# Kernel optimization log

Measured on AMD Instinct MI355X. Metric: run time of the kernel, lower is better.

## Reference

```python
import jax, jax.numpy as jnp
import numpy as np

B, L, NV = 16, 512, 64
D = 512
PATCH_LEN, STRIDE, PADDING = 16, 8, 8
N_PATCH = (L - PATCH_LEN) // STRIDE + 2  # 64
PRED = 192
MEM = 8192
TOPK = 8
NHEAD = 4
NORM_CONST = 0.4
HEAD_NF = D * N_PATCH


def _pos_emb(n, d):
    pos = np.arange(n)[:, None].astype(np.float32)
    div = np.exp(np.arange(0, d, 2).astype(np.float32) * (-np.log(10000.0) / d))
    pe = np.zeros((n, d), np.float32)
    pe[:, 0::2] = np.sin(pos * div)
    pe[:, 1::2] = np.cos(pos * div)
    return jnp.asarray(pe)

POS = _pos_emb(N_PATCH, D)


def gelu(x):
    return jax.nn.gelu(x, approximate=False)  # torch nn.GELU default = exact erf


def setup_inputs() -> dict:
    key = jax.random.key(0)
    ks = jax.random.split(key, 16)
    s = lambda i, shape, scale=0.02: jax.random.normal(ks[i], shape, jnp.float32) * scale
    return dict(
        x_enc=jax.random.normal(ks[0], (B, L, NV), jnp.float32),
        W_val=s(1, (PATCH_LEN, D), 0.05),
        mem_bank=s(2, (MEM, D), 1.0),
        W_m1=s(3, (D, 2 * D)), b_m1=jnp.zeros((2 * D,), jnp.float32),
        W_m2=s(4, (2 * D, D)), b_m2=jnp.zeros((D,), jnp.float32),
        W_q=s(5, (D, D)), b_q=jnp.zeros((D,), jnp.float32),
        W_k=s(6, (D, D)), b_k=jnp.zeros((D,), jnp.float32),
        W_v=s(7, (D, D)), b_v=jnp.zeros((D,), jnp.float32),
        W_o=s(8, (D, D)), b_o=jnp.zeros((D,), jnp.float32),
        W_g1=s(9, (2 * D, D)), b_g1=jnp.zeros((D,), jnp.float32),
        W_g2=s(10, (D, 2)), b_g2=jnp.zeros((2,), jnp.float32),
        W_h=s(11, (HEAD_NF, PRED)), b_h=jnp.zeros((PRED,), jnp.float32),
        W_f1=s(12, (PRED, 2 * PRED)), b_f1=jnp.zeros((2 * PRED,), jnp.float32),
        W_f2=s(13, (2 * PRED, PRED)), b_f2=jnp.zeros((PRED,), jnp.float32),
    )


def reference(x_enc, W_val, mem_bank, W_m1, b_m1, W_m2, b_m2,
              W_q, b_q, W_k, b_k, W_v, b_v, W_o, b_o,
              W_g1, b_g1, W_g2, b_g2, W_h, b_h, W_f1, b_f1, W_f2, b_f2):
    # instance normalization over the time axis (means detached in torch)
    means = jax.lax.stop_gradient(jnp.mean(x_enc, axis=1, keepdims=True))
    xc = x_enc - means
    stdev = jnp.sqrt(jnp.var(xc, axis=1, keepdims=True) + 1e-5) / NORM_CONST
    x = xc / stdev                                              # [B, L, NV]

    # patch embedding: replication pad at end, unfold, linear + sinusoidal pos
    xt = jnp.transpose(x, (0, 2, 1))                            # [B, NV, L]
    xt = jnp.concatenate([xt, jnp.repeat(xt[..., -1:], PADDING, axis=-1)], axis=-1)
    win = (jnp.arange(N_PATCH) * STRIDE)[:, None] + jnp.arange(PATCH_LEN)  # [N, P]
    patches = xt[..., win].reshape(B * NV, N_PATCH, PATCH_LEN)  # [BN, N, P]
    emb = patches @ W_val + POS                                 # [BN, N, D]

    # local memory: mean-pooled query -> matmul similarity -> top-k gather -> MLP
    qflat = jnp.mean(emb, axis=1)                               # [BN, D]
    sim = qflat @ mem_bank.T                                    # [BN, MEM]
    _, idx = jax.lax.top_k(sim, TOPK)                           # [BN, K]
    retr = mem_bank[idx]                                        # [BN, K, D]
    h = gelu(retr @ W_m1 + b_m1) @ W_m2 + b_m2
    local = jnp.mean(h, axis=1, keepdims=True) + emb            # [BN, N, D]

    # global memory: multihead self-attention (4 heads, batch_first)
    dh = D // NHEAD
    heads = lambda t: t.reshape(B * NV, N_PATCH, NHEAD, dh).transpose(0, 2, 1, 3)
    q = heads(emb @ W_q + b_q)
    k = heads(emb @ W_k + b_k)
    v = heads(emb @ W_v + b_v)
    att = jax.nn.softmax(jnp.einsum('bhqd,bhkd->bhqk', q, k) / jnp.sqrt(jnp.float32(dh)), axis=-1)
    glob = jnp.einsum('bhqk,bhkd->bhqd', att, v).transpose(0, 2, 1, 3).reshape(B * NV, N_PATCH, D)
    glob = glob @ W_o + b_o                                     # [BN, N, D]

    # gated fusion of local/global memory
    comb = jnp.concatenate([local, glob], axis=-1)              # [BN, N, 2D]
    gate = jax.nn.softmax(gelu(comb @ W_g1 + b_g1) @ W_g2 + b_g2, axis=-1)
    mem = gate[..., 0:1] * local + gate[..., 1:2] * glob        # [BN, N, D]

    # flatten -> memory head -> fusion layer with residual
    flat = mem.reshape(B * NV, HEAD_NF)
    mh = (flat @ W_h + b_h).reshape(B, NV, PRED)
    pred = gelu(gelu(mh @ W_f1 + b_f1) @ W_f2 + b_f2) + mh
    pred = jnp.transpose(pred, (0, 2, 1))                       # [B, PRED, NV]

    # denormalize
    return pred * stdev + means
```

## Files before the change

### kernel.cpp

```cpp
#include <hip/hip_runtime.h>
#include <stdint.h>

#define DEV __device__ __forceinline__

typedef uint16_t u16;
typedef __bf16 bf16x8 __attribute__((ext_vector_type(8)));
typedef float f32x4 __attribute__((ext_vector_type(4)));
typedef u16 u16x8 __attribute__((ext_vector_type(8)));
typedef u16 u16x4 __attribute__((ext_vector_type(4)));

DEV float bf2f(u16 v) { return __uint_as_float(((uint32_t)v) << 16); }
DEV u16 f2bf(float f) {
  uint32_t u = __float_as_uint(f);
  u += 0x7fffu + ((u >> 16) & 1u);
  return (u16)(u >> 16);
}
DEV float gelu_f(float x) { return 0.5f * x * (1.0f + erff(x * 0.7071067811865475f)); }

DEV void gload_lds16(const u16* g, u16* l) {
  __builtin_amdgcn_global_load_lds(
      (const __attribute__((address_space(1))) void*)g,
      (__attribute__((address_space(3))) void*)l, 16, 0, 0);
}

struct __align__(16) Scratch {
  float POSb[64 * 512];
  float meanv[1024];
  float stdv[1024];
  float mh[1024 * 192];
  int idxB[8192];
  float qflat[1024 * 512];
  float gatel[65536 * 2];
  u16 hmeanB[1024 * 512];
  u16 gmeanB[1024 * 1024];
  u16 WqT[512 * 512];
  u16 WkT[512 * 512];
  u16 WvT[512 * 512];
  u16 WoT[512 * 512];
  u16 Wm1T[1024 * 512];
  u16 Wm2T[512 * 1024];
  u16 Wg1T[512 * 1024];
  u16 WhT[256 * 32768];
  u16 memdupB[8192 * 1536];
  u16 embh[65536 * 512];
  u16 qb[65536 * 512];
  u16 kb[65536 * 512];
  u16 vb[65536 * 512];
};
__device__ Scratch g_s;

__global__ __launch_bounds__(256) void zerof_kernel(float* __restrict__ p, int n) {
  int t = blockIdx.x * 256 + threadIdx.x;
  if (t < n) p[t] = 0.f;
}
__global__ __launch_bounds__(256) void zerou_kernel(u16* __restrict__ p, int n) {
  int t = blockIdx.x * 256 + threadIdx.x;
  if (t < n) p[t] = 0;
}

__global__ __launch_bounds__(256) void pos_kernel(float* __restrict__ POS) {
  int n = blockIdx.x;
  int i = threadIdx.x;
  float div = expf((float)(2 * i) * (-9.210340371976184f / 512.0f));
  float arg = (float)n * div;
  POS[n * 512 + 2 * i] = sinf(arg);
  POS[n * 512 + 2 * i + 1] = cosf(arg);
}

__global__ __launch_bounds__(256) void stats_kernel(const float* __restrict__ x_enc,
                                                    float* __restrict__ meanv,
                                                    float* __restrict__ stdv) {
  int b = blockIdx.x;
  int v = threadIdx.x & 63;
  int g = threadIdx.x >> 6;
  float s = 0.f, s2 = 0.f;
  for (int l = g; l < 512; l += 4) {
    float x = x_enc[((long)b * 512 + l) * 64 + v];
    s += x; s2 += x * x;
  }
  __shared__ float sh[2][4][64];
  sh[0][g][v] = s; sh[1][g][v] = s2;
  __syncthreads();
  if (g == 0) {
    s = sh[0][0][v] + sh[0][1][v] + sh[0][2][v] + sh[0][3][v];
    s2 = sh[1][0][v] + sh[1][1][v] + sh[1][2][v] + sh[1][3][v];
    float mu = s * (1.f / 512.f);
    float var = s2 * (1.f / 512.f) - mu * mu;
    meanv[b * 64 + v] = mu;
    stdv[b * 64 + v] = sqrtf(var + 1e-5f) * 2.5f;
  }
}

__global__ __launch_bounds__(256) void transpose_kernel(const float* __restrict__ in,
                                                        u16* __restrict__ out, int R, int C) {
  __shared__ u16 t[32][33];
  int bx = blockIdx.x * 32;
  int by = blockIdx.y * 32;
  int tx = threadIdx.x & 31, ty = threadIdx.x >> 5;
  for (int i = ty; i < 32; i += 8) t[i][tx] = f2bf(in[(long)(by + i) * C + bx + tx]);
  __syncthreads();
  for (int i = ty; i < 32; i += 8) out[(long)(bx + i) * R + by + tx] = t[tx][i];
}

__global__ __launch_bounds__(256) void emb_kernel(const float* __restrict__ x_enc,
                                                  const float* __restrict__ W_val,
                                                  const float* __restrict__ POS,
                                                  const float* __restrict__ meanv,
                                                  const float* __restrict__ stdv,
                                                  u16* __restrict__ embh,
                                                  float* __restrict__ qflat) {
  int bn = blockIdx.x;
  int b = bn >> 6, v = bn & 63;
  int tid = threadIdx.x;
  __shared__ __align__(16) float wv[16 * 512];
  __shared__ __align__(16) float pt[64 * 16];
  for (int i = tid; i < 8192; i += 256) wv[i] = W_val[i];
  float mu = meanv[bn];
  float inv = 1.f / stdv[bn];
  for (int i = tid; i < 1024; i += 256) {
    int n = i >> 4, p = i & 15;
    int l = n * 8 + p; if (l > 511) l = 511;
    pt[i] = (x_enc[((long)b * 512 + l) * 64 + v] - mu) * inv;
  }
  __syncthreads();
  float qs0 = 0.f, qs1 = 0.f;
  int d0 = tid, d1 = tid + 256;
  for (int n = 0; n < 64; ++n) {
    float a0 = POS[n * 512 + d0], a1 = POS[n * 512 + d1];
#pragma unroll
    for (int p = 0; p < 16; ++p) {
      float pv = pt[n * 16 + p];
      a0 += pv * wv[p * 512 + d0];
      a1 += pv * wv[p * 512 + d1];
    }
    long base = ((long)bn * 64 + n) * 512;
    embh[base + d0] = f2bf(a0);
    embh[base + d1] = f2bf(a1);
    qs0 += a0; qs1 += a1;
  }
  qflat[(long)bn * 512 + d0] = qs0 * (1.f / 64.f);
  qflat[(long)bn * 512 + d1] = qs1 * (1.f / 64.f);
}

__global__ __launch_bounds__(256) void qsplit_kernel(const float* __restrict__ qflat,
                                                     u16* __restrict__ qsC) {
  int t = blockIdx.x * 256 + threadIdx.x;
  int bn = t >> 9, d = t & 511;
  float q = qflat[t];
  u16 hi = f2bf(q);
  u16 lo = f2bf(q - bf2f(hi));
  long base = (long)bn * 1536;
  qsC[base + d] = hi;
  qsC[base + 512 + d] = lo;
  qsC[base + 1024 + d] = hi;
}

__global__ __launch_bounds__(256) void memdup_kernel(const float* __restrict__ mb,
                                                     u16* __restrict__ md) {
  int t = blockIdx.x * 256 + threadIdx.x;
  int n = t >> 9, k = t & 511;
  float m = mb[t];
  u16 hi = f2bf(m);
  u16 lo = f2bf(m - bf2f(hi));
  long base = (long)n * 1536;
  md[base + k] = hi;
  md[base + 512 + k] = hi;
  md[base + 1024 + k] = lo;
}

template <int EPI>
__global__ __launch_bounds__(256) void gemm_nt(const u16* __restrict__ Ag,
                                               const u16* __restrict__ Bt,
                                               const float* __restrict__ bias,
                                               void* __restrict__ C,
                                               int lda, int ldb, int K, int Nreal, int ldc) {
  __shared__ __align__(16) u16 As[128 * 64];
  __shared__ __align__(16) u16 Bs[128 * 64];
  const int tid = threadIdx.x;
  const long bm = (long)blockIdx.x * 128;
  const long bnn = (long)blockIdx.y * 128;
  const long koff = (long)blockIdx.z * K;
  const int lane = tid & 63;
  const int w = tid >> 6;
  const int wm = (w & 1) * 64;
  const int wn = (w >> 1) * 64;
  const int r16 = lane & 15;
  const int q4 = lane >> 4;

  f32x4 acc[4][4] = {};

  const u16* ap[4];
  const u16* bp[4];
  u16* al[4];
  u16* bl[4];
#pragma unroll
  for (int j = 0; j < 4; ++j) {
    int cid = (j * 4 + w) * 64 + lane;
    int r = cid >> 3;
    int g = (cid & 7) ^ (r & 7);
    ap[j] = Ag + (bm + r) * lda + koff + g * 8;
    bp[j] = Bt + (bnn + r) * ldb + koff + g * 8;
    al[j] = As + cid * 8;
    bl[j] = Bs + cid * 8;
  }

  for (int k0 = 0; k0 < K; k0 += 64) {
#pragma unroll
    for (int j = 0; j < 4; ++j) gload_lds16(ap[j] + k0, al[j]);
#pragma unroll
    for (int j = 0; j < 4; ++j) gload_lds16(bp[j] + k0, bl[j]);
    __syncthreads();
#pragma unroll
    for (int sub = 0; sub < 2; ++sub) {
      const int gg = q4 + sub * 4;
      bf16x8 av[4], bv[4];
#pragma unroll
      for (int i = 0; i < 4; ++i) {
        int r = wm + i * 16 + r16;
        av[i] = *reinterpret_cast<const bf16x8*>(As + (r * 8 + (gg ^ (r & 7))) * 8);
      }
#pragma unroll
      for (int j2 = 0; j2 < 4; ++j2) {
        int r = wn + j2 * 16 + r16;
        bv[j2] = *reinterpret_cast<const bf16x8*>(Bs + (r * 8 + (gg ^ (r & 7))) * 8);
      }
#pragma unroll
      for (int i = 0; i < 4; ++i)
#pragma unroll
        for (int j2 = 0; j2 < 4; ++j2)
          acc[i][j2] = __builtin_amdgcn_mfma_f32_16x16x32_bf16(av[i], bv[j2], acc[i][j2], 0, 0, 0);
    }
    __syncthreads();
  }

#pragma unroll
  for (int i = 0; i < 4; ++i)
#pragma unroll
    for (int j = 0; j < 4; ++j)
#pragma unroll
      for (int r = 0; r < 4; ++r) {
        long grow = bm + wm + i * 16 + q4 * 4 + r;
        int gcol = (int)bnn + wn + j * 16 + r16;
        float v = acc[i][j][r];
        if (gcol < Nreal) {
          if (EPI == 0 || EPI == 1) {
            v += bias[gcol];
            if (EPI == 1) v = gelu_f(v);
            ((u16*)C)[grow * ldc + gcol] = f2bf(v);
          } else if (EPI == 2) {
            atomicAdd((float*)C + grow * ldc + gcol, v);
          } else {
            ((float*)C)[grow * ldc + gcol] = v;
          }
        }
      }
}

DEV bool better(float v1, int i1, float v2, int i2) {
  return v1 > v2 || (v1 == v2 && i1 < i2);
}
__global__ __launch_bounds__(256) void topk_kernel(const float* __restrict__ sim,
                                                   int* __restrict__ idxout) {
  const int bn = blockIdx.x;
  const int tid = threadIdx.x;
  const float* row = sim + (long)bn * 8192;
  float bv[8]; int bi[8];
#pragma unroll
  for (int r = 0; r < 8; ++r) { bv[r] = -3.0e38f; bi[r] = 0x7fffffff; }
  for (int n = tid; n < 8192; n += 256) {
    float v = row[n];
    if (better(v, n, bv[7], bi[7])) {
      bv[7] = v; bi[7] = n;
      for (int r = 7; r > 0; --r) {
        if (!better(bv[r], bi[r], bv[r - 1], bi[r - 1])) break;
        float tv = bv[r]; bv[r] = bv[r - 1]; bv[r - 1] = tv;
        int ti = bi[r]; bi[r] = bi[r - 1]; bi[r - 1] = ti;
      }
    }
  }
  __shared__ float lv[256 * 8];
  __shared__ int li[256 * 8];
#pragma unroll
  for (int r = 0; r < 8; ++r) { lv[tid * 8 + r] = bv[r]; li[tid * 8 + r] = bi[r]; }
  __syncthreads();
  for (int step = 128; step >= 1; step >>= 1) {
    if (tid < step) {
      float av[8], xv[8]; int ai[8], xi[8];
#pragma unroll
      for (int r = 0; r < 8; ++r) {
        av[r] = lv[tid * 8 + r]; ai[r] = li[tid * 8 + r];
        xv[r] = lv[(tid + step) * 8 + r]; xi[r] = li[(tid + step) * 8 + r];
      }
      int ia = 0, ib = 0;
      float mv[8]; int mi[8];
#pragma unroll
      for (int r = 0; r < 8; ++r) {
        if (better(av[ia], ai[ia], xv[ib], xi[ib])) { mv[r] = av[ia]; mi[r] = ai[ia]; ++ia; }
        else { mv[r] = xv[ib]; mi[r] = xi[ib]; ++ib; }
      }
#pragma unroll
      for (int r = 0; r < 8; ++r) { lv[tid * 8 + r] = mv[r]; li[tid * 8 + r] = mi[r]; }
    }
    __syncthreads();
  }
  if (tid < 8) idxout[bn * 8 + tid] = li[tid];
}

__global__ __launch_bounds__(256) void gather_kernel(const float* __restrict__ mb,
                                                     const int* __restrict__ idx,
                                                     u16* __restrict__ retrB) {
  int t = blockIdx.x * 256 + threadIdx.x;
  int m = t >> 6;
  int c8 = (t & 63) * 8;
  long r = idx[m];
  if (r < 0) r = 0;
  if (r > 8191) r = 8191;
  const float* src = mb + r * 512 + c8;
  u16* dst = retrB + (long)m * 512 + c8;
#pragma unroll
  for (int z = 0; z < 8; ++z) dst[z] = f2bf(src[z]);
}

__global__ __launch_bounds__(256) void gmean_kernel(const u16* __restrict__ hid,
                                                    u16* __restrict__ gmeanB) {
  int t = blockIdx.x * 256 + threadIdx.x;
  int bn = t >> 10, j = t & 1023;
  float s = 0.f;
#pragma unroll
  for (int k = 0; k < 8; ++k) s += bf2f(hid[(long)(bn * 8 + k) * 1024 + j]);
  gmeanB[t] = f2bf(s * 0.125f);
}

__global__ __launch_bounds__(256) void attn_kernel(u16* __restrict__ qb,
                                                   const u16* __restrict__ kb,
                                                   const u16* __restrict__ vb) {
  __shared__ __align__(16) u16 smem[26752];
  u16* Qs = smem;
  u16* Ks = smem + 8704;
  float* ss = (float*)(smem + 8704);
  u16* ps = smem;
  u16* Vb = smem + 17408;
  float* red = (float*)(smem + 25728);
  const int bn = blockIdx.x, h = blockIdx.y;
  const int tid = threadIdx.x;
  const int lane = tid & 63, w = tid >> 6;
  const int r16 = lane & 15, q4 = lane >> 4;
  const long base = (long)bn * 64 * 512 + h * 128;

  for (int c = tid; c < 1024; c += 256) {
    int r = c >> 4, c8 = (c & 15) * 8;
    u16x8 vq = *(const u16x8*)(qb + base + (long)r * 512 + c8);
    u16x8 vk = *(const u16x8*)(kb + base + (long)r * 512 + c8);
    u16x8 vv = *(const u16x8*)(vb + base + (long)r * 512 + c8);
    *(u16x8*)(Qs + r * 136 + c8) = vq;
    *(u16x8*)(Ks + r * 136 + c8) = vk;
    int kt = r >> 5, q4t = (r >> 3) & 3, e = r & 7;
    int nt = c8 >> 4, rb = c8 & 15;
    int vbase = (nt * 2 + kt) * 520 + (q4t * 16 + rb) * 8 + e;
#pragma unroll
    for (int z = 0; z < 8; ++z) Vb[vbase + z * 8] = vv[z];
  }
  __syncthreads();

  const int m0 = w * 16;
  f32x4 accS[4] = {};
#pragma unroll
  for (int k0 = 0; k0 < 128; k0 += 32) {
    bf16x8 av = *(const bf16x8*)(Qs + (m0 + r16) * 136 + k0 + q4 * 8);
#pragma unroll
    for (int j = 0; j < 4; ++j) {
      bf16x8 bvf = *(const bf16x8*)(Ks + (j * 16 + r16) * 136 + k0 + q4 * 8);
      accS[j] = __builtin_amdgcn_mfma_f32_16x16x32_bf16(av, bvf, accS[j], 0, 0, 0);
    }
  }
  __syncthreads();
  const float scale = 0.08838834764831845f;
#pragma unroll
  for (int j = 0; j < 4; ++j)
#pragma unroll
    for (int r = 0; r < 4; ++r)
      ss[(m0 + q4 * 4 + r) * 66 + j * 16 + r16] = accS[j][r] * scale;
  __syncthreads();

  {
    int r = tid >> 2, p = tid & 3;
    float* row = ss + r * 66 + p * 16;
    float mx = -3.0e38f;
#pragma unroll
    for (int c2 = 0; c2 < 16; ++c2) mx = fmaxf(mx, row[c2]);
    red[r * 4 + p] = mx;
    __syncthreads();
    float m4 = fmaxf(fmaxf(red[r * 4], red[r * 4 + 1]),
                     fmaxf(red[r * 4 + 2], red[r * 4 + 3]));
    float s = 0.f;
#pragma unroll
    for (int c2 = 0; c2 < 16; ++c2) {
      float e = expf(row[c2] - m4);
      row[c2] = e;
      s += e;
    }
    red[256 + r * 4 + p] = s;
    __syncthreads();
    float inv = 1.f / (red[256 + r * 4] + red[256 + r * 4 + 1] +
                       red[256 + r * 4 + 2] + red[256 + r * 4 + 3]);
    u16x8 o0, o1;
#pragma unroll
    for (int z = 0; z < 8; ++z) {
      o0[z] = f2bf(row[z] * inv);
      o1[z] = f2bf(row[8 + z] * inv);
    }
    *(u16x8*)(ps + r * 72 + p * 16) = o0;
    *(u16x8*)(ps + r * 72 + p * 16 + 8) = o1;
  }
  __syncthreads();

  bf16x8 av0 = *(const bf16x8*)(ps + (m0 + r16) * 72 + q4 * 8);
  bf16x8 av1 = *(const bf16x8*)(ps + (m0 + r16) * 72 + 32 + q4 * 8);
#pragma unroll
  for (int nt = 0; nt < 8; ++nt) {
    f32x4 accO = {};
    bf16x8 bv0 = *(const bf16x8*)(Vb + (nt * 2 + 0) * 520 + lane * 8);
    bf16x8 bv1 = *(const bf16x8*)(Vb + (nt * 2 + 1) * 520 + lane * 8);
    accO = __builtin_amdgcn_mfma_f32_16x16x32_bf16(av0, bv0, accO, 0, 0, 0);
    accO = __builtin_amdgcn_mfma_f32_16x16x32_bf16(av1, bv1, accO, 0, 0, 0);
    int d = nt * 16 + r16;
#pragma unroll
    for (int r = 0; r < 4; ++r) {
      int i = m0 + q4 * 4 + r;
      qb[base + (long)i * 512 + d] = f2bf(accO[r]);
    }
  }
}

__global__ __launch_bounds__(256) void local_kernel(u16* __restrict__ embh,
                                                    const u16* __restrict__ hmeanB) {
  long t = (long)blockIdx.x * 256 + threadIdx.x;
  long m = t >> 9;
  int d = (int)(t & 511);
  int bn = (int)(m >> 6);
  embh[t] = f2bf(bf2f(hmeanB[(long)bn * 512 + d]) + bf2f(embh[t]));
}

__global__ __launch_bounds__(256) void gemm_cat(const u16* __restrict__ A1,
                                                const u16* __restrict__ A2,
                                                const u16* __restrict__ Bt,
                                                const float* __restrict__ bias,
                                                u16* __restrict__ C) {
  __shared__ __align__(16) u16 As[128 * 64];
  __shared__ __align__(16) u16 Bs[128 * 64];
  const int tid = threadIdx.x;
  const long bm = (long)blockIdx.x * 128;
  const long bnn = (long)blockIdx.y * 128;
  const int lane = tid & 63;
  const int w = tid >> 6;
  const int wm = (w & 1) * 64;
  const int wn = (w >> 1) * 64;
  const int r16 = lane & 15;
  const int q4 = lane >> 4;

  f32x4 acc[4][4] = {};

  const u16* ap1[4];
  const u16* ap2[4];
  const u16* bp[4];
  u16* al[4];
  u16* bl[4];
#pragma unroll
  for (int j = 0; j < 4; ++j) {
    int cid = (j * 4 + w) * 64 + lane;
    int r = cid >> 3;
    int g = (cid & 7) ^ (r & 7);
    ap1[j] = A1 + (bm + r) * 512 + g * 8;
    ap2[j] = A2 + (bm + r) * 512 + g * 8;
    bp[j] = Bt + (bnn + r) * 1024 + g * 8;
    al[j] = As + cid * 8;
    bl[j] = Bs + cid * 8;
  }

  for (int k0 = 0; k0 < 1024; k0 += 64) {
    if (k0 < 512) {
#pragma unroll
      for (int j = 0; j < 4; ++j) gload_lds16(ap1[j] + k0, al[j]);
    } else {
#pragma unroll
      for (int j = 0; j < 4; ++j) gload_lds16(ap2[j] + (k0 - 512), al[j]);
    }
#pragma unroll
    for (int j = 0; j < 4; ++j) gload_lds16(bp[j] + k0, bl[j]);
    __syncthreads();
#pragma unroll
    for (int sub = 0; sub < 2; ++sub) {
      const int gg = q4 + sub * 4;
      bf16x8 av[4], bv[4];
#pragma unroll
      for (int i = 0; i < 4; ++i) {
        int r = wm + i * 16 + r16;
        av[i] = *reinterpret_cast<const bf16x8*>(As + (r * 8 + (gg ^ (r & 7))) * 8);
      }
#pragma unroll
      for (int j2 = 0; j2 < 4; ++j2) {
        int r = wn + j2 * 16 + r16;
        bv[j2] = *reinterpret_cast<const bf16x8*>(Bs + (r * 8 + (gg ^ (r & 7))) * 8);
      }
#pragma unroll
      for (int i = 0; i < 4; ++i)
#pragma unroll
        for (int j2 = 0; j2 < 4; ++j2)
          acc[i][j2] = __builtin_amdgcn_mfma_f32_16x16x32_bf16(av[i], bv[j2], acc[i][j2], 0, 0, 0);
    }
    __syncthreads();
  }

#pragma unroll
  for (int i = 0; i < 4; ++i)
#pragma unroll
    for (int j = 0; j < 4; ++j)
#pragma unroll
      for (int r = 0; r < 4; ++r) {
        long grow = bm + wm + i * 16 + q4 * 4 + r;
        int gcol = (int)bnn + wn + j * 16 + r16;
        float v = acc[i][j][r] + bias[gcol];
        C[grow * 512 + gcol] = f2bf(gelu_f(v));
      }
}

__global__ __launch_bounds__(256) void g2_kernel(const u16* __restrict__ h1b,
                                                 const float* __restrict__ W_g2,
                                                 const float* __restrict__ b_g2,
                                                 float* __restrict__ gatel) {
  int m = blockIdx.x * 4 + (threadIdx.x >> 6);
  int lane = threadIdx.x & 63;
  const u16* row = h1b + (long)m * 512;
  float a0 = 0.f, a1 = 0.f;
  for (int i = lane; i < 512; i += 64) {
    float h = bf2f(row[i]);
    a0 += h * W_g2[i * 2];
    a1 += h * W_g2[i * 2 + 1];
  }
  for (int off = 32; off; off >>= 1) {
    a0 += __shfl_down(a0, off);
    a1 += __shfl_down(a1, off);
  }
  if (lane == 0) {
    a0 += b_g2[0];
    a1 += b_g2[1];
    float mx = fmaxf(a0, a1);
    float e0 = expf(a0 - mx), e1 = expf(a1 - mx);
    float inv = 1.f / (e0 + e1);
    gatel[(long)m * 2] = e0 * inv;
    gatel[(long)m * 2 + 1] = e1 * inv;
  }
}

__global__ __launch_bounds__(256) void memc_kernel(const u16* __restrict__ localB,
                                                   const u16* __restrict__ globB,
                                                   const float* __restrict__ gatel,
                                                   u16* __restrict__ memB) {
  long t = (long)blockIdx.x * 256 + threadIdx.x;
  long m = t >> 9;
  float loc = bf2f(localB[t]);
  float gl = bf2f(globB[t]);
  float g0 = gatel[m * 2], g1 = gatel[m * 2 + 1];
  memB[t] = f2bf(g0 * loc + g1 * gl);
}

__global__ __launch_bounds__(256) void fusion_kernel(const float* __restrict__ mh,
                                                     const float* __restrict__ b_h,
                                                     const float* __restrict__ W_f1,
                                                     const float* __restrict__ b_f1,
                                                     const float* __restrict__ W_f2,
                                                     const float* __restrict__ b_f2,
                                                     const float* __restrict__ meanv,
                                                     const float* __restrict__ stdv,
                                                     float* __restrict__ out) {
  int bn = blockIdx.x;
  int tid = threadIdx.x;
  __shared__ float mrow[192];
  __shared__ float h1[384];
  if (tid < 192) mrow[tid] = mh[(long)bn * 192 + tid] + b_h[tid];
  __syncthreads();
  for (int j = tid; j < 384; j += 256) {
    float a = b_f1[j];
    for (int i = 0; i < 192; ++i) a += mrow[i] * W_f1[i * 384 + j];
    h1[j] = gelu_f(a);
  }
  __syncthreads();
  if (tid < 192) {
    float a = b_f2[tid];
    for (int j = 0; j < 384; ++j) a += h1[j] * W_f2[j * 192 + tid];
    float o = gelu_f(a) + mrow[tid];
    int b = bn >> 6, v = bn & 63;
    out[((long)b * 192 + tid) * 64 + v] = o * stdv[bn] + meanv[bn];
  }
}

extern "C" void kernel_launch(void* const* d_in, const int* in_sizes, int n_in,
                              void* d_out, int out_size, void* d_ws, size_t ws_size,
                              hipStream_t stream) {
  (void)in_sizes; (void)n_in; (void)out_size; (void)d_ws; (void)ws_size;
  const float* x_enc = (const float*)d_in[0];
  const float* W_val = (const float*)d_in[1];
  const float* mem_bank = (const float*)d_in[2];
  const float* W_m1 = (const float*)d_in[3];
  const float* b_m1 = (const float*)d_in[4];
  const float* W_m2 = (const float*)d_in[5];
  const float* b_m2 = (const float*)d_in[6];
  const float* W_q = (const float*)d_in[7];
  const float* b_q = (const float*)d_in[8];
  const float* W_k = (const float*)d_in[9];
  const float* b_k = (const float*)d_in[10];
  const float* W_v = (const float*)d_in[11];
  const float* b_v = (const float*)d_in[12];
  const float* W_o = (const float*)d_in[13];
  const float* b_o = (const float*)d_in[14];
  const float* W_g1 = (const float*)d_in[15];
  const float* b_g1 = (const float*)d_in[16];
  const float* W_g2 = (const float*)d_in[17];
  const float* b_g2 = (const float*)d_in[18];
  const float* W_h = (const float*)d_in[19];
  const float* b_h = (const float*)d_in[20];
  const float* W_f1 = (const float*)d_in[21];
  const float* b_f1 = (const float*)d_in[22];
  const float* W_f2 = (const float*)d_in[23];
  const float* b_f2 = (const float*)d_in[24];

  void* sp = nullptr;
  hipGetSymbolAddress(&sp, HIP_SYMBOL(g_s));
  Scratch* S = (Scratch*)sp;
  u16* qsC = S->vb;
  float* simB = (float*)S->qb;
  u16* retrB = S->kb;
  u16* hiddenB = S->kb + (size_t)4 * 1024 * 1024;

  pos_kernel<<<64, 256, 0, stream>>>(S->POSb);
  stats_kernel<<<16, 256, 0, stream>>>(x_enc, S->meanv, S->stdv);
  zerof_kernel<<<768, 256, 0, stream>>>(S->mh, 1024 * 192);
  zerou_kernel<<<8192, 256, 0, stream>>>(S->WhT + (size_t)192 * 32768, 64 * 32768);
  transpose_kernel<<<dim3(16, 16), 256, 0, stream>>>(W_q, S->WqT, 512, 512);
  transpose_kernel<<<dim3(16, 16), 256, 0, stream>>>(W_k, S->WkT, 512, 512);
  transpose_kernel<<<dim3(16, 16), 256, 0, stream>>>(W_v, S->WvT, 512, 512);
  transpose_kernel<<<dim3(16, 16), 256, 0, stream>>>(W_o, S->WoT, 512, 512);
  transpose_kernel<<<dim3(32, 16), 256, 0, stream>>>(W_m1, S->Wm1T, 512, 1024);
  transpose_kernel<<<dim3(16, 32), 256, 0, stream>>>(W_m2, S->Wm2T, 1024, 512);
  transpose_kernel<<<dim3(16, 32), 256, 0, stream>>>(W_g1, S->Wg1T, 1024, 512);
  transpose_kernel<<<dim3(6, 1024), 256, 0, stream>>>(W_h, S->WhT, 32768, 192);
  memdup_kernel<<<16384, 256, 0, stream>>>(mem_bank, S->memdupB);

  emb_kernel<<<1024, 256, 0, stream>>>(x_enc, W_val, S->POSb, S->meanv, S->stdv,
                                       S->embh, S->qflat);
  qsplit_kernel<<<2048, 256, 0, stream>>>(S->qflat, qsC);
  gemm_nt<3><<<dim3(8, 64), 256, 0, stream>>>(qsC, S->memdupB, nullptr, simB,
                                              1536, 1536, 1536, 8192, 8192);
  topk_kernel<<<1024, 256, 0, stream>>>(simB, S->idxB);
  gather_kernel<<<2048, 256, 0, stream>>>(mem_bank, S->idxB, retrB);
  gemm_nt<1><<<dim3(64, 8), 256, 0, stream>>>(retrB, S->Wm1T, b_m1, hiddenB,
                                              512, 512, 512, 1024, 1024);
  gmean_kernel<<<4096, 256, 0, stream>>>(hiddenB, S->gmeanB);
  gemm_nt<0><<<dim3(8, 4), 256, 0, stream>>>(S->gmeanB, S->Wm2T, b_m2, S->hmeanB,
                                             1024, 1024, 1024, 512, 512);
  gemm_nt<0><<<dim3(512, 4), 256, 0, stream>>>(S->embh, S->WqT, b_q, S->qb,
                                               512, 512, 512, 512, 512);
  gemm_nt<0><<<dim3(512, 4), 256, 0, stream>>>(S->embh, S->WkT, b_k, S->kb,
                                               512, 512, 512, 512, 512);
  gemm_nt<0><<<dim3(512, 4), 256, 0, stream>>>(S->embh, S->WvT, b_v, S->vb,
                                               512, 512, 512, 512, 512);
  local_kernel<<<131072, 256, 0, stream>>>(S->embh, S->hmeanB);
  attn_kernel<<<dim3(1024, 4), 256, 0, stream>>>(S->qb, S->kb, S->vb);
  gemm_nt<0><<<dim3(512, 4), 256, 0, stream>>>(S->qb, S->WoT, b_o, S->kb,
                                               512, 512, 512, 512, 512);
  gemm_cat<<<dim3(512, 4), 256, 0, stream>>>(S->embh, S->kb, S->Wg1T, b_g1, S->vb);
  g2_kernel<<<16384, 256, 0, stream>>>(S->vb, W_g2, b_g2, S->gatel);
  memc_kernel<<<131072, 256, 0, stream>>>(S->embh, S->kb, S->gatel, S->qb);
  gemm_nt<2><<<dim3(8, 2, 16), 256, 0, stream>>>(S->qb, S->WhT, nullptr, S->mh,
                                                 32768, 32768, 2048, 192, 192);
  fusion_kernel<<<1024, 256, 0, stream>>>(S->mh, b_h, W_f1, b_f1, W_f2, b_f2,
                                          S->meanv, S->stdv, (float*)d_out);
}
```

Baseline: 1.129 ms.

## Fuse Q/K/V projections into one GEMM and swap grid axes for N-major tiles

Concatenates Wq/Wk/Wv into one transposed weight and bias buffer so a single GEMM writes an interleaved [M,1536] QKV buffer. This replaces three launches that each re-read the embedding activations. Downstream kernels (attention, out-projection, gated fusion, g2, memc) now take strided leading dimensions into that shared buffer. The GEMM grids are also swapped so blockIdx.x walks N tiles, letting consecutive blocks share the same A rows in cache; the trade-off is a wider 1536-column row stride and rewritten scratch aliasing.

```diff
diff --git a/kernel.cpp b/kernel.cpp
--- a/kernel.cpp
+++ b/kernel.cpp
@@ -7,7 +7,6 @@
 typedef __bf16 bf16x8 __attribute__((ext_vector_type(8)));
 typedef float f32x4 __attribute__((ext_vector_type(4)));
 typedef u16 u16x8 __attribute__((ext_vector_type(8)));
-typedef u16 u16x4 __attribute__((ext_vector_type(4)));
 
 DEV float bf2f(u16 v) { return __uint_as_float(((uint32_t)v) << 16); }
 DEV u16 f2bf(float f) {
@@ -31,11 +30,10 @@
   int idxB[8192];
   float qflat[1024 * 512];
   float gatel[65536 * 2];
+  float bqkv[1536];
   u16 hmeanB[1024 * 512];
   u16 gmeanB[1024 * 1024];
-  u16 WqT[512 * 512];
-  u16 WkT[512 * 512];
-  u16 WvT[512 * 512];
+  u16 WqkvT[1536 * 512];
   u16 WoT[512 * 512];
   u16 Wm1T[1024 * 512];
   u16 Wm2T[512 * 1024];
@@ -43,9 +41,7 @@
   u16 WhT[256 * 32768];
   u16 memdupB[8192 * 1536];
   u16 embh[65536 * 512];
-  u16 qb[65536 * 512];
-  u16 kb[65536 * 512];
-  u16 vb[65536 * 512];
+  u16 qkvb[65536 * 1536];
 };
 __device__ Scratch g_s;
 
@@ -56,6 +52,13 @@
 __global__ __launch_bounds__(256) void zerou_kernel(u16* __restrict__ p, int n) {
   int t = blockIdx.x * 256 + threadIdx.x;
   if (t < n) p[t] = 0;
+}
+__global__ __launch_bounds__(256) void biasqkv_kernel(const float* __restrict__ bq,
+                                                      const float* __restrict__ bk,
+                                                      const float* __restrict__ bv,
+                                                      float* __restrict__ o) {
+  int t = blockIdx.x * 256 + threadIdx.x;
+  o[t] = t < 512 ? bq[t] : (t < 1024 ? bk[t - 512] : bv[t - 1024]);
 }
 
 __global__ __launch_bounds__(256) void pos_kernel(float* __restrict__ POS) {
@@ -177,8 +180,8 @@
   __shared__ __align__(16) u16 As[128 * 64];
   __shared__ __align__(16) u16 Bs[128 * 64];
   const int tid = threadIdx.x;
-  const long bm = (long)blockIdx.x * 128;
-  const long bnn = (long)blockIdx.y * 128;
+  const long bnn = (long)blockIdx.x * 128;
+  const long bm = (long)blockIdx.y * 128;
   const long koff = (long)blockIdx.z * K;
   const int lane = tid & 63;
   const int w = tid >> 6;
@@ -331,9 +334,7 @@
   gmeanB[t] = f2bf(s * 0.125f);
 }
 
-__global__ __launch_bounds__(256) void attn_kernel(u16* __restrict__ qb,
-                                                   const u16* __restrict__ kb,
-                                                   const u16* __restrict__ vb) {
+__global__ __launch_bounds__(256) void attn_kernel(u16* __restrict__ qkvb) {
   __shared__ __align__(16) u16 smem[26752];
   u16* Qs = smem;
   u16* Ks = smem + 8704;
@@ -345,13 +346,13 @@
   const int tid = threadIdx.x;
   const int lane = tid & 63, w = tid >> 6;
   const int r16 = lane & 15, q4 = lane >> 4;
-  const long base = (long)bn * 64 * 512 + h * 128;
+  const long base = (long)bn * 64 * 1536 + h * 128;
 
   for (int c = tid; c < 1024; c += 256) {
     int r = c >> 4, c8 = (c & 15) * 8;
-    u16x8 vq = *(const u16x8*)(qb + base + (long)r * 512 + c8);
-    u16x8 vk = *(const u16x8*)(kb + base + (long)r * 512 + c8);
-    u16x8 vv = *(const u16x8*)(vb + base + (long)r * 512 + c8);
+    u16x8 vq = *(const u16x8*)(qkvb + base + (long)r * 1536 + c8);
+    u16x8 vk = *(const u16x8*)(qkvb + base + (long)r * 1536 + 512 + c8);
+    u16x8 vv = *(const u16x8*)(qkvb + base + (long)r * 1536 + 1024 + c8);
     *(u16x8*)(Qs + r * 136 + c8) = vq;
     *(u16x8*)(Ks + r * 136 + c8) = vk;
     int kt = r >> 5, q4t = (r >> 3) & 3, e = r & 7;
@@ -427,7 +428,7 @@
 #pragma unroll
     for (int r = 0; r < 4; ++r) {
       int i = m0 + q4 * 4 + r;
-      qb[base + (long)i * 512 + d] = f2bf(accO[r]);
+      qkvb[base + (long)i * 1536 + d] = f2bf(accO[r]);
     }
   }
 }
@@ -445,12 +446,13 @@
                                                 const u16* __restrict__ A2,
                                                 const u16* __restrict__ Bt,
                                                 const float* __restrict__ bias,
-                                                u16* __restrict__ C) {
+                                                u16* __restrict__ C,
+                                                int lda1, int lda2, int ldc) {
   __shared__ __align__(16) u16 As[128 * 64];
   __shared__ __align__(16) u16 Bs[128 * 64];
   const int tid = threadIdx.x;
-  const long bm = (long)blockIdx.x * 128;
-  const long bnn = (long)blockIdx.y * 128;
+  const long bnn = (long)blockIdx.x * 128;
+  const long bm = (long)blockIdx.y * 128;
   const int lane = tid & 63;
   const int w = tid >> 6;
   const int wm = (w & 1) * 64;
@@ -470,8 +472,8 @@
     int cid = (j * 4 + w) * 64 + lane;
     int r = cid >> 3;
     int g = (cid & 7) ^ (r & 7);
-    ap1[j] = A1 + (bm + r) * 512 + g * 8;
-    ap2[j] = A2 + (bm + r) * 512 + g * 8;
+    ap1[j] = A1 + (bm + r) * lda1 + g * 8;
+    ap2[j] = A2 + (bm + r) * lda2 + g * 8;
     bp[j] = Bt + (bnn + r) * 1024 + g * 8;
     al[j] = As + cid * 8;
     bl[j] = Bs + cid * 8;
@@ -520,17 +522,17 @@
         long grow = bm + wm + i * 16 + q4 * 4 + r;
         int gcol = (int)bnn + wn + j * 16 + r16;
         float v = acc[i][j][r] + bias[gcol];
-        C[grow * 512 + gcol] = f2bf(gelu_f(v));
+        C[grow * ldc + gcol] = f2bf(gelu_f(v));
       }
 }
 
 __global__ __launch_bounds__(256) void g2_kernel(const u16* __restrict__ h1b,
                                                  const float* __restrict__ W_g2,
                                                  const float* __restrict__ b_g2,
-                                                 float* __restrict__ gatel) {
+                                                 float* __restrict__ gatel, int ld) {
   int m = blockIdx.x * 4 + (threadIdx.x >> 6);
   int lane = threadIdx.x & 63;
-  const u16* row = h1b + (long)m * 512;
+  const u16* row = h1b + (long)m * ld;
   float a0 = 0.f, a1 = 0.f;
   for (int i = lane; i < 512; i += 64) {
     float h = bf2f(row[i]);
@@ -552,16 +554,16 @@
   }
 }
 
-__global__ __launch_bounds__(256) void memc_kernel(const u16* __restrict__ localB,
-                                                   const u16* __restrict__ globB,
-                                                   const float* __restrict__ gatel,
-                                                   u16* __restrict__ memB) {
+__global__ __launch_bounds__(256) void memc_kernel(u16* __restrict__ embh,
+                                                   const u16* __restrict__ qkvb,
+                                                   const float* __restrict__ gatel) {
   long t = (long)blockIdx.x * 256 + threadIdx.x;
   long m = t >> 9;
-  float loc = bf2f(localB[t]);
-  float gl = bf2f(globB[t]);
+  int d = (int)(t & 511);
+  float loc = bf2f(embh[t]);
+  float gl = bf2f(qkvb[m * 1536 + 512 + d]);
   float g0 = gatel[m * 2], g1 = gatel[m * 2 + 1];
-  memB[t] = f2bf(g0 * loc + g1 * gl);
+  embh[t] = f2bf(g0 * loc + g1 * gl);
 }
 
 __global__ __launch_bounds__(256) void fusion_kernel(const float* __restrict__ mh,
@@ -627,18 +629,19 @@
   void* sp = nullptr;
   hipGetSymbolAddress(&sp, HIP_SYMBOL(g_s));
   Scratch* S = (Scratch*)sp;
-  u16* qsC = S->vb;
-  float* simB = (float*)S->qb;
-  u16* retrB = S->kb;
-  u16* hiddenB = S->kb + (size_t)4 * 1024 * 1024;
+  float* simB = (float*)S->qkvb;
+  u16* qsC = S->qkvb + (size_t)16 * 1024 * 1024;
+  u16* retrB = S->qkvb + (size_t)18 * 1024 * 1024;
+  u16* hiddenB = S->qkvb + (size_t)24 * 1024 * 1024;
 
   pos_kernel<<<64, 256, 0, stream>>>(S->POSb);
   stats_kernel<<<16, 256, 0, stream>>>(x_enc, S->meanv, S->stdv);
   zerof_kernel<<<768, 256, 0, stream>>>(S->mh, 1024 * 192);
   zerou_kernel<<<8192, 256, 0, stream>>>(S->WhT + (size_t)192 * 32768, 64 * 32768);
-  transpose_kernel<<<dim3(16, 16), 256, 0, stream>>>(W_q, S->WqT, 512, 512);
-  transpose_kernel<<<dim3(16, 16), 256, 0, stream>>>(W_k, S->WkT, 512, 512);
-  transpose_kernel<<<dim3(16, 16), 256, 0, stream>>>(W_v, S->WvT, 512, 512);
+  biasqkv_kernel<<<6, 256, 0, stream>>>(b_q, b_k, b_v, S->bqkv);
+  transpose_kernel<<<dim3(16, 16), 256, 0, stream>>>(W_q, S->WqkvT, 512, 512);
+  transpose_kernel<<<dim3(16, 16), 256, 0, stream>>>(W_k, S->WqkvT + 512 * 512, 512, 512);
+  transpose_kernel<<<dim3(16, 16), 256, 0, stream>>>(W_v, S->WqkvT + 2 * 512 * 512, 512, 512);
   transpose_kernel<<<dim3(16, 16), 256, 0, stream>>>(W_o, S->WoT, 512, 512);
   transpose_kernel<<<dim3(32, 16), 256, 0, stream>>>(W_m1, S->Wm1T, 512, 1024);
   transpose_kernel<<<dim3(16, 32), 256, 0, stream>>>(W_m2, S->Wm2T, 1024, 512);
@@ -649,29 +652,26 @@
   emb_kernel<<<1024, 256, 0, stream>>>(x_enc, W_val, S->POSb, S->meanv, S->stdv,
                                        S->embh, S->qflat);
   qsplit_kernel<<<2048, 256, 0, stream>>>(S->qflat, qsC);
-  gemm_nt<3><<<dim3(8, 64), 256, 0, stream>>>(qsC, S->memdupB, nullptr, simB,
+  gemm_nt<3><<<dim3(64, 8), 256, 0, stream>>>(qsC, S->memdupB, nullptr, simB,
                                               1536, 1536, 1536, 8192, 8192);
   topk_kernel<<<1024, 256, 0, stream>>>(simB, S->idxB);
   gather_kernel<<<2048, 256, 0, stream>>>(mem_bank, S->idxB, retrB);
-  gemm_nt<1><<<dim3(64, 8), 256, 0, stream>>>(retrB, S->Wm1T, b_m1, hiddenB,
+  gemm_nt<1><<<dim3(8, 64), 256, 0, stream>>>(retrB, S->Wm1T, b_m1, hiddenB,
                                               512, 512, 512, 1024, 1024);
   gmean_kernel<<<4096, 256, 0, stream>>>(hiddenB, S->gmeanB);
-  gemm_nt<0><<<dim3(8, 4), 256, 0, stream>>>(S->gmeanB, S->Wm2T, b_m2, S->hmeanB,
+  gemm_nt<0><<<dim3(4, 8), 256, 0, stream>>>(S->gmeanB, S->Wm2T, b_m2, S->hmeanB,
                                              1024, 1024, 1024, 512, 512);
-  gemm_nt<0><<<dim3(512, 4), 256, 0, stream>>>(S->embh, S->WqT, b_q, S->qb,
-                                               512, 512, 512, 512, 512);
-  gemm_nt<0><<<dim3(512, 4), 256, 0, stream>>>(S->embh, S->WkT, b_k, S->kb,
-                                               512, 512, 512, 512, 512);
-  gemm_nt<0><<<dim3(512, 4), 256, 0, stream>>>(S->embh, S->WvT, b_v, S->vb,
-                                               512, 512, 512, 512, 512);
+  gemm_nt<0><<<dim3(12, 512), 256, 0, stream>>>(S->embh, S->WqkvT, S->bqkv, S->qkvb,
+                                                512, 512, 512, 1536, 1536);
   local_kernel<<<131072, 256, 0, stream>>>(S->embh, S->hmeanB);
-  attn_kernel<<<dim3(1024, 4), 256, 0, stream>>>(S->qb, S->kb, S->vb);
-  gemm_nt<0><<<dim3(512, 4), 256, 0, stream>>>(S->qb, S->WoT, b_o, S->kb,
-                                               512, 512, 512, 512, 512);
-  gemm_cat<<<dim3(512, 4), 256, 0, stream>>>(S->embh, S->kb, S->Wg1T, b_g1, S->vb);
-  g2_kernel<<<16384, 256, 0, stream>>>(S->vb, W_g2, b_g2, S->gatel);
-  memc_kernel<<<131072, 256, 0, stream>>>(S->embh, S->kb, S->gatel, S->qb);
-  gemm_nt<2><<<dim3(8, 2, 16), 256, 0, stream>>>(S->qb, S->WhT, nullptr, S->mh,
+  attn_kernel<<<dim3(1024, 4), 256, 0, stream>>>(S->qkvb);
+  gemm_nt<0><<<dim3(4, 512), 256, 0, stream>>>(S->qkvb, S->WoT, b_o, S->qkvb + 512,
+                                               1536, 512, 512, 512, 1536);
+  gemm_cat<<<dim3(4, 512), 256, 0, stream>>>(S->embh, S->qkvb + 512, S->Wg1T, b_g1,
+                                             S->qkvb + 1024, 512, 1536, 1536);
+  g2_kernel<<<16384, 256, 0, stream>>>(S->qkvb + 1024, W_g2, b_g2, S->gatel, 1536);
+  memc_kernel<<<131072, 256, 0, stream>>>(S->embh, S->qkvb, S->gatel);
+  gemm_nt<2><<<dim3(2, 8, 16), 256, 0, stream>>>(S->embh, S->WhT, nullptr, S->mh,
                                                  32768, 32768, 2048, 192, 192);
   fusion_kernel<<<1024, 256, 0, stream>>>(S->mh, b_h, W_f1, b_f1, W_f2, b_f2,
                                           S->meanv, S->stdv, (float*)d_out);
```

Measured after the change: 1.103 ms. -2.3%, faster.
